# Optimization experiments

Measured on AMD Instinct MI355X. Metric: run time of the kernel, lower is better.

The kernel has to match this reference:

```python
import jax, jax.numpy as jnp
import numpy as np

N = 100000   # nodes
E = 1000000  # edges (before self-loops)
D = 64       # input_dim
H = 64       # hidden_dim
OUT = 8      # output_dim
G = 128      # num graphs in batch


def setup_inputs() -> dict:
    key = jax.random.key(0)
    ks = jax.random.split(key, 8)
    x = jax.random.normal(ks[0], (N, D), jnp.float32)
    edge_index = jax.random.randint(ks[1], (2, E), 0, N)
    edge_attr = jax.random.uniform(ks[2], (E,), jnp.float32)
    batch = jnp.sort(jax.random.randint(ks[3], (N,), 0, G))
    W1 = jax.random.normal(ks[4], (H, D), jnp.float32) / np.float32(np.sqrt(D))
    b1 = jnp.zeros((H,), jnp.float32)
    W2 = jax.random.normal(ks[5], (OUT, H), jnp.float32) / np.float32(np.sqrt(H))
    b2 = jnp.zeros((OUT,), jnp.float32)
    Wopt = jax.random.normal(ks[6], (1, H), jnp.float32) / np.float32(np.sqrt(H))
    bopt = jnp.zeros((1,), jnp.float32)
    return dict(x=x, edge_index=edge_index, edge_attr=edge_attr, batch=batch,
                W1=W1, b1=b1, W2=W2, b2=b2, Wopt=Wopt, bopt=bopt,
                num_graphs=G)


def gcn_conv(x, edge_index, edge_attr, W, b):
    n = x.shape[0]
    loop = jnp.arange(n)
    # add_self_loops with fill_value=1.0
    row = jnp.concatenate([edge_index[0], loop])
    col = jnp.concatenate([edge_index[1], loop])
    ea = jnp.concatenate([edge_attr, jnp.ones((n,), x.dtype)])
    # degree over row (source); >=1 because of self-loops
    deg = jax.ops.segment_sum(jnp.ones(row.shape, x.dtype), row, num_segments=n)
    dis = deg ** -0.5
    norm = dis[row] * dis[col]
    # message: edge_attr * x_j * norm, gathered from source row
    msg = (ea * norm)[:, None] * x[row]          # [E+N, D]
    aggr = jax.ops.segment_sum(msg, col, num_segments=n)  # scatter-add at target
    return aggr @ W.T + b                        # update: linear


def reference(x, edge_index, edge_attr, batch, W1, b1, W2, b2, Wopt, bopt, num_graphs):
    h = jnp.tanh(gcn_conv(x, edge_index, edge_attr, W1, b1))
    out = jax.nn.sigmoid(h @ W2.T + b2)          # [N, OUT]
    counts = jax.ops.segment_sum(jnp.ones((h.shape[0],), h.dtype), batch,
                                 num_segments=num_graphs)
    gemb = jax.ops.segment_sum(h, batch, num_segments=num_graphs)
    gemb = gemb / jnp.maximum(counts, 1.0)[:, None]  # global_mean_pool
    optimal = jax.nn.sigmoid(gemb @ Wopt.T + bopt)   # [G, 1]
    return (out, optimal)
```

## Files before the change

### kernel.cpp

```cpp
#include <hip/hip_runtime.h>
#include <math.h>
#include <stdint.h>

#define DD 64
#define HH 64
#define OUTD 8
#define NG 128
#define PSPLIT 8
#define NB 512
#define RSH 8
#define RMSK 255
#define CAPD 3072
#define BIN_CHUNK 4096
#define BT 1024

typedef short short8 __attribute__((ext_vector_type(8)));
typedef float f32x4 __attribute__((ext_vector_type(4)));

__device__ __forceinline__ float sigmoidf_(float v) { return 1.0f / (1.0f + __expf(-v)); }
__device__ __forceinline__ unsigned short f2bf(float f) {
    unsigned u = __float_as_uint(f);
    unsigned r = u + 0x7FFFu + ((u >> 16) & 1u);
    return (unsigned short)(r >> 16);
}
__device__ __forceinline__ float bf2f(unsigned short b) {
    return __uint_as_float(((unsigned)b) << 16);
}
__device__ __forceinline__ float bflo(unsigned q) { return __uint_as_float(q << 16); }
__device__ __forceinline__ float bfhi(unsigned q) { return __uint_as_float(q & 0xFFFF0000u); }

__device__ __forceinline__ int lbound_(const int* __restrict__ batch, int N, int g) {
    int lo = 0, hi = N;
    while (lo < hi) { int m = (lo + hi) >> 1; if (batch[m] < g) lo = m + 1; else hi = m; }
    return lo;
}

__global__ __launch_bounds__(BT)
void bin_xcvt_kernel(const int* __restrict__ ei, const float* __restrict__ ea,
                     int* gcur, int* scur, int2* __restrict__ dreg,
                     unsigned char* __restrict__ sreg, int E, int nbin,
                     const float4* __restrict__ x4, uint4* __restrict__ xbf, int n8) {
    if (blockIdx.x >= nbin) {
        int i = (blockIdx.x - nbin) * BT + threadIdx.x;
        if (i < n8) {
            float4 a = x4[i * 2], b = x4[i * 2 + 1];
            uint4 o;
            o.x = (unsigned)f2bf(a.x) | ((unsigned)f2bf(a.y) << 16);
            o.y = (unsigned)f2bf(a.z) | ((unsigned)f2bf(a.w) << 16);
            o.z = (unsigned)f2bf(b.x) | ((unsigned)f2bf(b.y) << 16);
            o.w = (unsigned)f2bf(b.z) | ((unsigned)f2bf(b.w) << 16);
            xbf[i] = o;
        }
        return;
    }
    __shared__ int dcnt[NB], scnt[NB], dbase[NB], sbase[NB];
    int t = threadIdx.x;
    for (int j = t; j < NB; j += BT) { dcnt[j] = 0; scnt[j] = 0; }
    __syncthreads();
    int e0 = blockIdx.x * BIN_CHUNK;
    int lim = min(BIN_CHUNK, E - e0);
    int rv0 = 0, rv1 = 0, rv2 = 0, rv3 = 0;
    int cv0 = 0, cv1 = 0, cv2 = 0, cv3 = 0;
    float av0 = 0, av1 = 0, av2 = 0, av3 = 0;
    {
        int i;
        i = t;            if (i < lim) { rv0 = ei[e0+i]; cv0 = ei[E+e0+i]; av0 = ea[e0+i];
                                         atomicAdd(&dcnt[cv0 >> RSH], 1); atomicAdd(&scnt[rv0 >> RSH], 1); }
        i = t + BT;       if (i < lim) { rv1 = ei[e0+i]; cv1 = ei[E+e0+i]; av1 = ea[e0+i];
                                         atomicAdd(&dcnt[cv1 >> RSH], 1); atomicAdd(&scnt[rv1 >> RSH], 1); }
        i = t + 2 * BT;   if (i < lim) { rv2 = ei[e0+i]; cv2 = ei[E+e0+i]; av2 = ea[e0+i];
                                         atomicAdd(&dcnt[cv2 >> RSH], 1); atomicAdd(&scnt[rv2 >> RSH], 1); }
        i = t + 3 * BT;   if (i < lim) { rv3 = ei[e0+i]; cv3 = ei[E+e0+i]; av3 = ea[e0+i];
                                         atomicAdd(&dcnt[cv3 >> RSH], 1); atomicAdd(&scnt[rv3 >> RSH], 1); }
    }
    __syncthreads();
    for (int j = t; j < NB; j += BT) {
        int dc = dcnt[j], sc = scnt[j];
        dbase[j] = dc ? atomicAdd(&gcur[j], dc) : 0;
        sbase[j] = sc ? atomicAdd(&scur[j], sc) : 0;
        dcnt[j] = 0; scnt[j] = 0;
    }
    __syncthreads();
    #define EMIT(RR, CC, AA, II) do { \
        if ((II) < lim) { \
            int b_ = (CC) >> RSH, cl_ = (CC) & RMSK; \
            int pos_ = dbase[b_] + atomicAdd(&dcnt[b_], 1); \
            if (pos_ < CAPD) dreg[(size_t)b_ * CAPD + pos_] = make_int2((RR) | (cl_ << 20), __float_as_int(AA)); \
            int sb_ = (RR) >> RSH; \
            int sp_ = sbase[sb_] + atomicAdd(&scnt[sb_], 1); \
            if (sp_ < CAPD) sreg[(size_t)sb_ * CAPD + sp_] = (unsigned char)((RR) & RMSK); \
        } } while (0)
    EMIT(rv0, cv0, av0, t);
    EMIT(rv1, cv1, av1, t + BT);
    EMIT(rv2, cv2, av2, t + 2 * BT);
    EMIT(rv3, cv3, av3, t + 3 * BT);
    #undef EMIT
}

__global__ __launch_bounds__(256)
void deg_kernel(const unsigned char* __restrict__ sreg, const int* __restrict__ scur,
                float* __restrict__ dis, int N) {
    __shared__ int cnt[256];
    int t = threadIdx.x, b = blockIdx.x;
    cnt[t] = 0;
    __syncthreads();
    int n = min(scur[b], CAPD);
    const unsigned char* p = sreg + (size_t)b * CAPD;
    for (int i = t; i < n; i += 256) atomicAdd(&cnt[p[i]], 1);
    __syncthreads();
    int node = (b << RSH) + t;
    if (node < N) dis[node] = rsqrtf(1.0f + (float)cnt[t]);
}

__global__ __launch_bounds__(256)
void csr_kernel(int2* __restrict__ dreg, const int* __restrict__ gcur,
                const float* __restrict__ dis,
                int* __restrict__ colstart, int* __restrict__ colcnt, int N) {
    __shared__ int2 recs[CAPD];
    __shared__ int cnt[256], offs_s[256], sc[256];
    int t = threadIdx.x, b = blockIdx.x;
    int n = min(gcur[b], CAPD);
    size_t base = (size_t)b * CAPD;
    for (int i = t; i < n; i += 256) recs[i] = dreg[base + i];
    cnt[t] = 0;
    __syncthreads();
    for (int i = t; i < n; i += 256) atomicAdd(&cnt[recs[i].x >> 20], 1);
    __syncthreads();
    int my = cnt[t];
    sc[t] = my;
    __syncthreads();
    for (int off = 1; off < 256; off <<= 1) {
        int v = (t >= off) ? sc[t - off] : 0;
        __syncthreads();
        sc[t] += v;
        __syncthreads();
    }
    int ex = sc[t] - my;
    offs_s[t] = ex;
    int node = (b << RSH) + t;
    if (node < N) { colstart[node] = (int)(base + ex); colcnt[node] = my; }
    cnt[t] = 0;
    __syncthreads();
    for (int i = t; i < n; i += 256) {
        int2 rc = recs[i];
        int cl = rc.x >> 20;
        int r = rc.x & 0xFFFFF;
        float coef = __int_as_float(rc.y) * dis[r] * dis[(b << RSH) + cl];
        int pos = offs_s[cl] + atomicAdd(&cnt[cl], 1);
        dreg[base + pos] = make_int2(r, __float_as_int(coef));
    }
}

__global__ __launch_bounds__(256)
void gather_kernel(const int2* __restrict__ recs,
                   const int* __restrict__ colstart, const int* __restrict__ colcnt,
                   const float* __restrict__ dis,
                   const unsigned short* __restrict__ xbf,
                   unsigned* __restrict__ axb, int N) {
    int wid = blockIdx.x * 4 + (threadIdx.x >> 6);
    int l = threadIdx.x & 63;
    int half = l >> 5, d2 = l & 31;
    int node = wid * 2 + half;
    bool v = node < N;
    float s = v ? dis[node] : 0.f;
    unsigned xv = v ? *(const unsigned*)(xbf + (size_t)node * DD + 2 * d2) : 0u;
    float a0 = s * s * bflo(xv);
    float a1 = s * s * bfhi(xv);
    float b0 = 0.f, b1 = 0.f;
    int cnt = v ? colcnt[node] : 0;
    const int2* p = recs + (v ? colstart[node] : 0);
    int k = 0;
    for (; k + 4 <= cnt; k += 4) {
        int2 r0 = p[k], r1 = p[k + 1], r2 = p[k + 2], r3 = p[k + 3];
        unsigned q0 = *(const unsigned*)(xbf + (size_t)r0.x * DD + 2 * d2);
        unsigned q1 = *(const unsigned*)(xbf + (size_t)r1.x * DD + 2 * d2);
        unsigned q2 = *(const unsigned*)(xbf + (size_t)r2.x * DD + 2 * d2);
        unsigned q3 = *(const unsigned*)(xbf + (size_t)r3.x * DD + 2 * d2);
        float c0 = __int_as_float(r0.y), c1 = __int_as_float(r1.y);
        float c2 = __int_as_float(r2.y), c3 = __int_as_float(r3.y);
        a0 += c0 * bflo(q0); a1 += c0 * bfhi(q0);
        b0 += c1 * bflo(q1); b1 += c1 * bfhi(q1);
        a0 += c2 * bflo(q2); a1 += c2 * bfhi(q2);
        b0 += c3 * bflo(q3); b1 += c3 * bfhi(q3);
    }
    for (; k < cnt; ++k) {
        int2 r0 = p[k];
        unsigned q0 = *(const unsigned*)(xbf + (size_t)r0.x * DD + 2 * d2);
        float c0 = __int_as_float(r0.y);
        a0 += c0 * bflo(q0); a1 += c0 * bfhi(q0);
    }
    if (v) {
        float v0 = a0 + b0, v1 = a1 + b1;
        axb[(size_t)node * (DD / 2) + d2] = (unsigned)f2bf(v0) | ((unsigned)f2bf(v1) << 16);
    }
}

__global__ __launch_bounds__(256)
void head_kernel(const unsigned short* __restrict__ axb,
                 const float* __restrict__ W1, const float* __restrict__ b1,
                 const float* __restrict__ W2, const float* __restrict__ b2,
                 unsigned short* __restrict__ hb, float* __restrict__ outp, int N) {
    __shared__ __align__(16) float htile[4][16][68];
    int tid = threadIdx.x;
    int l = tid & 63, w = tid >> 6;
    int col = l & 15, kg = l >> 4;
    int half = l >> 5, d2 = l & 31;

    short8 w1f[4][2];
    #pragma unroll
    for (int ct = 0; ct < 4; ++ct)
        #pragma unroll
        for (int kt = 0; kt < 2; ++kt) {
            const float* src = W1 + (16 * ct + col) * DD + 32 * kt + 8 * kg;
            short8 f;
            #pragma unroll
            for (int j = 0; j < 8; ++j) f[j] = (short)f2bf(src[j]);
            w1f[ct][kt] = f;
        }
    short8 w2f[2];
    #pragma unroll
    for (int kt = 0; kt < 2; ++kt) {
        short8 f;
        #pragma unroll
        for (int j = 0; j < 8; ++j)
            f[j] = (col < OUTD) ? (short)f2bf(W2[col * HH + 32 * kt + 8 * kg + j]) : (short)0;
        w2f[kt] = f;
    }
    float b1v[4];
    #pragma unroll
    for (int ct = 0; ct < 4; ++ct) b1v[ct] = b1[16 * ct + col];
    float b2v = (col < OUTD) ? b2[col] : 0.f;

    int ngrp = (N + 15) >> 4;
    int g = blockIdx.x * 4 + w;
    bool act = g < ngrp;
    int base = act ? g * 16 : 0;
    int rr = min(base + col, N - 1);

    short8 af[2];
    #pragma unroll
    for (int kt = 0; kt < 2; ++kt)
        af[kt] = *(const short8*)(axb + (size_t)rr * DD + 32 * kt + 8 * kg);

    #pragma unroll
    for (int ct = 0; ct < 4; ++ct) {
        f32x4 acc = {0.f, 0.f, 0.f, 0.f};
        acc = __builtin_amdgcn_mfma_f32_16x16x32_bf16(af[0], w1f[ct][0], acc, 0, 0, 0);
        acc = __builtin_amdgcn_mfma_f32_16x16x32_bf16(af[1], w1f[ct][1], acc, 0, 0, 0);
        #pragma unroll
        for (int jr = 0; jr < 4; ++jr) {
            float v = acc[jr] + b1v[ct];
            float ez = __expf(2.f * v);
            htile[w][4 * kg + jr][16 * ct + col] = (ez - 1.f) / (ez + 1.f);
        }
    }
    __syncthreads();

    #pragma unroll
    for (int it = 0; it < 8; ++it) {
        int node = base + 2 * it + half;
        if (act && node < N) {
            float h0 = htile[w][2 * it + half][2 * d2];
            float h1 = htile[w][2 * it + half][2 * d2 + 1];
            *(unsigned*)(hb + (size_t)node * HH + 2 * d2) =
                (unsigned)f2bf(h0) | ((unsigned)f2bf(h1) << 16);
        }
    }

    short8 hf[2];
    #pragma unroll
    for (int kt = 0; kt < 2; ++kt) {
        const float* src = &htile[w][col][32 * kt + 8 * kg];
        float4 lo = *(const float4*)src;
        float4 hi = *(const float4*)(src + 4);
        short8 f;
        f[0] = (short)f2bf(lo.x); f[1] = (short)f2bf(lo.y);
        f[2] = (short)f2bf(lo.z); f[3] = (short)f2bf(lo.w);
        f[4] = (short)f2bf(hi.x); f[5] = (short)f2bf(hi.y);
        f[6] = (short)f2bf(hi.z); f[7] = (short)f2bf(hi.w);
        hf[kt] = f;
    }
    f32x4 acc2 = {0.f, 0.f, 0.f, 0.f};
    acc2 = __builtin_amdgcn_mfma_f32_16x16x32_bf16(hf[0], w2f[0], acc2, 0, 0, 0);
    acc2 = __builtin_amdgcn_mfma_f32_16x16x32_bf16(hf[1], w2f[1], acc2, 0, 0, 0);
    if (act && col < OUTD) {
        #pragma unroll
        for (int jr = 0; jr < 4; ++jr) {
            int node = base + 4 * kg + jr;
            if (node < N) outp[(size_t)node * OUTD + col] = sigmoidf_(acc2[jr] + b2v);
        }
    }
}

__global__ void pool_kernel(const unsigned short* __restrict__ hb,
                            const int* __restrict__ batch, int N,
                            float* __restrict__ gemb) {
    int g = blockIdx.x / PSPLIT;
    int part = blockIdx.x % PSPLIT;
    int s = lbound_(batch, N, g);
    int e = lbound_(batch, N, g + 1);
    int tid = threadIdx.x;
    int hc = tid & 63, nl = tid >> 6;
    float sum = 0.0f;
    for (int n = s + part * 4 + nl; n < e; n += PSPLIT * 4)
        sum += bf2f(hb[(size_t)n * HH + hc]);
    __shared__ float red[4][HH];
    red[nl][hc] = sum;
    __syncthreads();
    if (nl == 0) {
        float v = red[0][hc] + red[1][hc] + red[2][hc] + red[3][hc];
        atomicAdd(&gemb[g * HH + hc], v);
    }
}

__global__ void optimal_kernel(const float* __restrict__ gemb,
                               const int* __restrict__ batch, int N,
                               const float* __restrict__ Wopt,
                               const float* __restrict__ bopt,
                               float* __restrict__ out2) {
    int g = blockIdx.x;
    int d = threadIdx.x;
    int s = lbound_(batch, N, g);
    int e = lbound_(batch, N, g + 1);
    float c = fmaxf((float)(e - s), 1.0f);
    float v = gemb[g * HH + d] / c * Wopt[d];
    #pragma unroll
    for (int off = 32; off > 0; off >>= 1) v += __shfl_down(v, off);
    if (d == 0) out2[g] = 1.0f / (1.0f + __expf(-(v + bopt[0])));
}

extern "C" void kernel_launch(void* const* d_in, const int* in_sizes, int n_in,
                              void* d_out, int out_size, void* d_ws, size_t ws_size,
                              hipStream_t stream) {
    const float* x     = (const float*)d_in[0];
    const int*   ei    = (const int*)d_in[1];
    const float* ea    = (const float*)d_in[2];
    const int*   batch = (const int*)d_in[3];
    const float* W1    = (const float*)d_in[4];
    const float* b1    = (const float*)d_in[5];
    const float* W2    = (const float*)d_in[6];
    const float* b2    = (const float*)d_in[7];
    const float* Wopt  = (const float*)d_in[8];
    const float* bopt  = (const float*)d_in[9];

    int N = in_sizes[0] / DD;
    int E = in_sizes[2];
    int nbins = (N + 255) >> 8;

    float* out  = (float*)d_out;
    float* out2 = out + (size_t)N * OUTD;

    char* p = (char*)d_ws;
    float* dis      = (float*)p;  p += (size_t)N * 4;
    int*   colstart = (int*)p;    p += (size_t)N * 4;
    int*   colcnt   = (int*)p;    p += (size_t)N * 4;
    float* gemb     = (float*)p;  p += (size_t)NG * HH * 4;
    int*   gcur     = (int*)p;    p += (size_t)NB * 4;
    int*   scur     = (int*)p;    p += (size_t)NB * 4;
    uintptr_t up = (uintptr_t)p; up = (up + 15) & ~(uintptr_t)15; p = (char*)up;
    int2* dreg = (int2*)p;        p += (size_t)nbins * CAPD * 8;
    unsigned char* sreg = (unsigned char*)p; p += (size_t)nbins * CAPD;
    up = (uintptr_t)p; up = (up + 15) & ~(uintptr_t)15; p = (char*)up;
    unsigned short* xbf = (unsigned short*)p; p += (size_t)N * DD * 2;
    unsigned* axb = (unsigned*)p; p += (size_t)N * (DD / 2) * 4;
    unsigned short* hb  = (unsigned short*)p;

    int n8 = N * DD / 8;
    int nbin = (E + BIN_CHUNK - 1) / BIN_CHUNK;
    int nxc = (n8 + BT - 1) / BT;

    hipMemsetAsync(gcur, 0, (size_t)NB * 8, stream);
    hipMemsetAsync(gemb, 0, (size_t)NG * HH * 4, stream);

    bin_xcvt_kernel<<<nbin + nxc, BT, 0, stream>>>(ei, ea, gcur, scur, dreg, sreg,
                                                   E, nbin,
                                                   (const float4*)x, (uint4*)xbf, n8);
    deg_kernel<<<nbins, 256, 0, stream>>>(sreg, scur, dis, N);
    csr_kernel<<<nbins, 256, 0, stream>>>(dreg, gcur, dis, colstart, colcnt, N);

    gather_kernel<<<(N + 7) / 8, 256, 0, stream>>>(dreg, colstart, colcnt, dis, xbf, axb, N);

    int ngrp = (N + 15) / 16;
    head_kernel<<<(ngrp + 3) / 4, 256, 0, stream>>>((const unsigned short*)axb,
                                                    W1, b1, W2, b2, hb, out, N);

    pool_kernel<<<NG * PSPLIT, 256, 0, stream>>>(hb, batch, N, gemb);
    optimal_kernel<<<NG, 64, 0, stream>>>(gemb, batch, N, Wopt, bopt, out2);
}
```

Baseline: 133.6 us.

## Widen gather to four nodes per wave, drop memsets and pool atomics

The gather kernel now processes four nodes per wavefront with 16 lanes each, loading 8-byte bf16 chunks per neighbor, and halves its grid. The two hipMemsetAsync calls are replaced by one tiny init kernel. The pooling atomics are replaced by per-part partial sums that the optimal kernel reduces. This cuts launch/memset overhead and atomic contention, and raises bytes per load in the gather, at the cost of fewer lanes in flight per node.

```diff
diff --git a/kernel.cpp b/kernel.cpp
--- a/kernel.cpp
+++ b/kernel.cpp
@@ -33,6 +33,10 @@
     int lo = 0, hi = N;
     while (lo < hi) { int m = (lo + hi) >> 1; if (batch[m] < g) lo = m + 1; else hi = m; }
     return lo;
+}
+
+__global__ void init_kernel(int* cur2) {
+    cur2[threadIdx.x] = 0;
 }
 
 __global__ __launch_bounds__(BT)
@@ -159,39 +163,41 @@
                    unsigned* __restrict__ axb, int N) {
     int wid = blockIdx.x * 4 + (threadIdx.x >> 6);
     int l = threadIdx.x & 63;
-    int half = l >> 5, d2 = l & 31;
-    int node = wid * 2 + half;
+    int q = l >> 4;
+    int d4 = l & 15;
+    int node = wid * 4 + q;
     bool v = node < N;
     float s = v ? dis[node] : 0.f;
-    unsigned xv = v ? *(const unsigned*)(xbf + (size_t)node * DD + 2 * d2) : 0u;
-    float a0 = s * s * bflo(xv);
-    float a1 = s * s * bfhi(xv);
-    float b0 = 0.f, b1 = 0.f;
+    uint2 xv = v ? *(const uint2*)(xbf + (size_t)node * DD + 4 * d4) : make_uint2(0u, 0u);
+    float s2 = s * s;
+    float a0 = s2 * bflo(xv.x), a1 = s2 * bfhi(xv.x);
+    float a2 = s2 * bflo(xv.y), a3 = s2 * bfhi(xv.y);
+    float b0 = 0.f, b1 = 0.f, b2 = 0.f, b3 = 0.f;
     int cnt = v ? colcnt[node] : 0;
     const int2* p = recs + (v ? colstart[node] : 0);
     int k = 0;
-    for (; k + 4 <= cnt; k += 4) {
-        int2 r0 = p[k], r1 = p[k + 1], r2 = p[k + 2], r3 = p[k + 3];
-        unsigned q0 = *(const unsigned*)(xbf + (size_t)r0.x * DD + 2 * d2);
-        unsigned q1 = *(const unsigned*)(xbf + (size_t)r1.x * DD + 2 * d2);
-        unsigned q2 = *(const unsigned*)(xbf + (size_t)r2.x * DD + 2 * d2);
-        unsigned q3 = *(const unsigned*)(xbf + (size_t)r3.x * DD + 2 * d2);
+    for (; k + 2 <= cnt; k += 2) {
+        int2 r0 = p[k], r1 = p[k + 1];
+        uint2 q0 = *(const uint2*)(xbf + (size_t)r0.x * DD + 4 * d4);
+        uint2 q1 = *(const uint2*)(xbf + (size_t)r1.x * DD + 4 * d4);
         float c0 = __int_as_float(r0.y), c1 = __int_as_float(r1.y);
-        float c2 = __int_as_float(r2.y), c3 = __int_as_float(r3.y);
-        a0 += c0 * bflo(q0); a1 += c0 * bfhi(q0);
-        b0 += c1 * bflo(q1); b1 += c1 * bfhi(q1);
-        a0 += c2 * bflo(q2); a1 += c2 * bfhi(q2);
-        b0 += c3 * bflo(q3); b1 += c3 * bfhi(q3);
-    }
-    for (; k < cnt; ++k) {
+        a0 += c0 * bflo(q0.x); a1 += c0 * bfhi(q0.x);
+        a2 += c0 * bflo(q0.y); a3 += c0 * bfhi(q0.y);
+        b0 += c1 * bflo(q1.x); b1 += c1 * bfhi(q1.x);
+        b2 += c1 * bflo(q1.y); b3 += c1 * bfhi(q1.y);
+    }
+    if (k < cnt) {
         int2 r0 = p[k];
-        unsigned q0 = *(const unsigned*)(xbf + (size_t)r0.x * DD + 2 * d2);
+        uint2 q0 = *(const uint2*)(xbf + (size_t)r0.x * DD + 4 * d4);
         float c0 = __int_as_float(r0.y);
-        a0 += c0 * bflo(q0); a1 += c0 * bfhi(q0);
+        a0 += c0 * bflo(q0.x); a1 += c0 * bfhi(q0.x);
+        a2 += c0 * bflo(q0.y); a3 += c0 * bfhi(q0.y);
     }
     if (v) {
-        float v0 = a0 + b0, v1 = a1 + b1;
-        axb[(size_t)node * (DD / 2) + d2] = (unsigned)f2bf(v0) | ((unsigned)f2bf(v1) << 16);
+        uint2 o;
+        o.x = (unsigned)f2bf(a0 + b0) | ((unsigned)f2bf(a1 + b1) << 16);
+        o.y = (unsigned)f2bf(a2 + b2) | ((unsigned)f2bf(a3 + b3) << 16);
+        *(uint2*)(axb + (size_t)node * (DD / 2) + 2 * d4) = o;
     }
 }
 
@@ -294,7 +300,7 @@
 
 __global__ void pool_kernel(const unsigned short* __restrict__ hb,
                             const int* __restrict__ batch, int N,
-                            float* __restrict__ gemb) {
+                            float* __restrict__ pp) {
     int g = blockIdx.x / PSPLIT;
     int part = blockIdx.x % PSPLIT;
     int s = lbound_(batch, N, g);
@@ -307,13 +313,12 @@
     __shared__ float red[4][HH];
     red[nl][hc] = sum;
     __syncthreads();
-    if (nl == 0) {
-        float v = red[0][hc] + red[1][hc] + red[2][hc] + red[3][hc];
-        atomicAdd(&gemb[g * HH + hc], v);
-    }
-}
-
-__global__ void optimal_kernel(const float* __restrict__ gemb,
+    if (nl == 0)
+        pp[((size_t)g * PSPLIT + part) * HH + hc] =
+            red[0][hc] + red[1][hc] + red[2][hc] + red[3][hc];
+}
+
+__global__ void optimal_kernel(const float* __restrict__ pp,
                                const int* __restrict__ batch, int N,
                                const float* __restrict__ Wopt,
                                const float* __restrict__ bopt,
@@ -323,7 +328,11 @@
     int s = lbound_(batch, N, g);
     int e = lbound_(batch, N, g + 1);
     float c = fmaxf((float)(e - s), 1.0f);
-    float v = gemb[g * HH + d] / c * Wopt[d];
+    float acc = 0.f;
+    #pragma unroll
+    for (int part = 0; part < PSPLIT; ++part)
+        acc += pp[((size_t)g * PSPLIT + part) * HH + d];
+    float v = acc / c * Wopt[d];
     #pragma unroll
     for (int off = 32; off > 0; off >>= 1) v += __shfl_down(v, off);
     if (d == 0) out2[g] = 1.0f / (1.0f + __expf(-(v + bopt[0])));
@@ -354,7 +363,7 @@
     float* dis      = (float*)p;  p += (size_t)N * 4;
     int*   colstart = (int*)p;    p += (size_t)N * 4;
     int*   colcnt   = (int*)p;    p += (size_t)N * 4;
-    float* gemb     = (float*)p;  p += (size_t)NG * HH * 4;
+    float* pp       = (float*)p;  p += (size_t)NG * PSPLIT * HH * 4;
     int*   gcur     = (int*)p;    p += (size_t)NB * 4;
     int*   scur     = (int*)p;    p += (size_t)NB * 4;
     uintptr_t up = (uintptr_t)p; up = (up + 15) & ~(uintptr_t)15; p = (char*)up;
@@ -369,21 +378,19 @@
     int nbin = (E + BIN_CHUNK - 1) / BIN_CHUNK;
     int nxc = (n8 + BT - 1) / BT;
 
-    hipMemsetAsync(gcur, 0, (size_t)NB * 8, stream);
-    hipMemsetAsync(gemb, 0, (size_t)NG * HH * 4, stream);
-
+    init_kernel<<<1, 2 * NB, 0, stream>>>(gcur);
     bin_xcvt_kernel<<<nbin + nxc, BT, 0, stream>>>(ei, ea, gcur, scur, dreg, sreg,
                                                    E, nbin,
                                                    (const float4*)x, (uint4*)xbf, n8);
     deg_kernel<<<nbins, 256, 0, stream>>>(sreg, scur, dis, N);
     csr_kernel<<<nbins, 256, 0, stream>>>(dreg, gcur, dis, colstart, colcnt, N);
 
-    gather_kernel<<<(N + 7) / 8, 256, 0, stream>>>(dreg, colstart, colcnt, dis, xbf, axb, N);
+    gather_kernel<<<(N + 15) / 16, 256, 0, stream>>>(dreg, colstart, colcnt, dis, xbf, axb, N);
 
     int ngrp = (N + 15) / 16;
     head_kernel<<<(ngrp + 3) / 4, 256, 0, stream>>>((const unsigned short*)axb,
                                                     W1, b1, W2, b2, hb, out, N);
 
-    pool_kernel<<<NG * PSPLIT, 256, 0, stream>>>(hb, batch, N, gemb);
-    optimal_kernel<<<NG, 64, 0, stream>>>(gemb, batch, N, Wopt, bopt, out2);
-}
+    pool_kernel<<<NG * PSPLIT, 256, 0, stream>>>(hb, batch, N, pp);
+    optimal_kernel<<<NG, 64, 0, stream>>>(pp, batch, N, Wopt, bopt, out2);
+}
```

Measured after the change: 128.1 us. -4.1%, faster.
